# Performance work log

Hardware: AMD Instinct MI355X
Metric: run time of the kernel (lower is better)

The kernel has to match this reference:

```python
import jax, jax.numpy as jnp
import numpy as np

N_NODES = 50000
N_EDGES = 800000
HC = 64      # hidden_channels
NG = 5       # num_gaussians
NF = 64      # num_filters
SL = 20      # short_len
NC = 2       # n_conv
Z_DIM = 2 * NF + SL  # 148
BN_EPS = 1e-5


def setup_inputs() -> dict:
    key = jax.random.key(0)
    ks = jax.random.split(key, 16)
    s = 0.05
    return {
        "h": jax.random.normal(ks[0], (N_NODES, HC), dtype=jnp.float32),
        "edge_index": jax.random.randint(ks[1], (2, N_EDGES), 0, N_NODES, dtype=jnp.int32),
        "edge_weight": jax.random.uniform(ks[2], (N_EDGES,), dtype=jnp.float32),
        "edge_attr": jax.random.uniform(ks[3], (N_EDGES, NG), dtype=jnp.float32),
        "lin0_w": jax.random.normal(ks[4], (HC, NF), dtype=jnp.float32) * s,
        "lin0_b": jnp.zeros((NF,), dtype=jnp.float32),
        "short_w": jax.random.normal(ks[5], (NG, SL), dtype=jnp.float32) * s,
        "short_b": jnp.zeros((SL,), dtype=jnp.float32),
        "linf_w": jax.random.normal(ks[6], (NC, Z_DIM, NF), dtype=jnp.float32) * s,
        "linf_b": jnp.zeros((NC, NF), dtype=jnp.float32),
        "lins_w": jax.random.normal(ks[7], (NC, Z_DIM, NF), dtype=jnp.float32) * s,
        "lins_b": jnp.zeros((NC, NF), dtype=jnp.float32),
        "bn_gamma": jnp.ones((NC, NF), dtype=jnp.float32),
        "bn_beta": jnp.zeros((NC, NF), dtype=jnp.float32),
        "data": 0,
    }


def reference(h, edge_index, edge_weight, edge_attr,
              lin0_w, lin0_b, short_w, short_b,
              linf_w, linf_b, lins_w, lins_b,
              bn_gamma, bn_beta, data):
    # lin0 + relu
    out = jax.nn.relu(h @ lin0_w + lin0_b)                      # [N, NF]
    # short edge-attr projection + relu
    ea = jax.nn.relu(edge_attr @ short_w + short_b)             # [E, SL]
    src = edge_index[0]  # x_j (source)
    dst = edge_index[1]  # x_i (target / aggregation index)
    n = out.shape[0]
    for l in range(NC):
        x_i = out[dst]                                          # [E, NF]
        x_j = out[src]                                          # [E, NF]
        z = jnp.concatenate([x_i, x_j, ea], axis=-1)            # [E, 148]
        msg = jax.nn.sigmoid(z @ linf_w[l] + linf_b[l]) * \
              jax.nn.softplus(z @ lins_w[l] + lins_b[l])        # [E, NF]
        agg = jax.ops.segment_sum(msg, dst, num_segments=n)     # [N, NF]
        # BatchNorm1d (training-mode batch stats, biased variance)
        mean = jnp.mean(agg, axis=0)
        var = jnp.mean((agg - mean) ** 2, axis=0)
        bn = (agg - mean) * jax.lax.rsqrt(var + BN_EPS) * bn_gamma[l] + bn_beta[l]
        conv_out = bn + out                                     # CGConv internal residual
        out = out + jax.nn.relu(conv_out)                       # _Interactions residual
    return out
```

## Files before the change

kernel.cpp:

```cpp
#include <hip/hip_runtime.h>
#include <hip/hip_bf16.h>

#define N_NODES 50000
#define N_EDGES 800000
#define SCAN_NB 49
#define EPW 32
#define EW_BLOCKS 6250

typedef __hip_bfloat16 bf16;
typedef unsigned int u32;
typedef unsigned short u16;
typedef _Float16 hh2 __attribute__((ext_vector_type(2)));

#if defined(__has_builtin)
#if __has_builtin(__builtin_amdgcn_fdot2)
#define HAVE_FDOT2 1
#endif
#endif

__device__ __forceinline__ float bfb(u32 b) { return __uint_as_float(b << 16); }

__device__ __forceinline__ u16 f2bf(float x) {
    bf16 a = __float2bfloat16(x);
    u16 u;
    __builtin_memcpy(&u, &a, 2);
    return u;
}

__device__ __forceinline__ hh2 pkrtz(float a, float b) {
    auto r = __builtin_amdgcn_cvt_pkrtz(a, b);
    hh2 o;
    __builtin_memcpy(&o, &r, 4);
    return o;
}

__device__ __forceinline__ float ldf(const void* p, long i, int f32) {
    if (f32) return ((const float*)p)[i];
    return bfb((u32)((const u16*)p)[i]);
}

__device__ __forceinline__ int detect_f32(const u32* g) { return g[0] == 0x3F800000u; }

__global__ __launch_bounds__(256) void k_front(const void* __restrict__ h,
        const void* __restrict__ w, const void* __restrict__ b,
        const u32* __restrict__ gr, u16* __restrict__ outw,
        const int* __restrict__ ei, int* __restrict__ cnt,
        int* __restrict__ tsum, u32* __restrict__ aggz) {
    int t = threadIdx.x;
    for (int i = blockIdx.x * 256 + t; i < N_NODES * 64; i += 1024 * 256)
        aggz[i] = 0;
    if (blockIdx.x >= 512) {
        __shared__ int lts[SCAN_NB];
        if (t < SCAN_NB) lts[t] = 0;
        __syncthreads();
        int bid = blockIdx.x - 512;
        for (int e = bid * 256 + t; e < N_EDGES; e += 512 * 256) {
            int dst = ei[N_EDGES + e];
            atomicAdd(&cnt[dst], 1);
            atomicAdd(&lts[dst >> 10], 1);
        }
        __syncthreads();
        if (t < SCAN_NB) atomicAdd(&tsum[t], lts[t]);
        return;
    }
    __shared__ float Wl[64 * 64];
    __shared__ float bl[64];
    __shared__ float hs[256];
    int f32 = detect_f32(gr);
    for (int i = t; i < 4096; i += 256) Wl[i] = ldf(w, i, f32);
    if (t < 64) bl[t] = ldf(b, t, f32);
    int c = t & 63, g = t >> 6;
    for (int chunk = blockIdx.x; chunk < N_NODES / 4; chunk += 512) {
        __syncthreads();
        int node0 = chunk * 4;
        hs[t] = ldf(h, (long)node0 * 64 + t, f32);
        __syncthreads();
        float acc = bl[c];
        #pragma unroll
        for (int k = 0; k < 64; ++k) acc = fmaf(hs[g * 64 + k], Wl[k * 64 + c], acc);
        outw[(node0 + g) * 64 + c] = f2bf(fmaxf(acc, 0.f));
    }
}

__global__ __launch_bounds__(1024) void k_scan(int* __restrict__ cnt,
        const int* __restrict__ tsum) {
    __shared__ int wsum[16];
    __shared__ int boff_s;
    int t = threadIdx.x, lane = t & 63, wv = t >> 6;
    if (wv == 0) {
        int v = (lane < SCAN_NB && lane < (int)blockIdx.x) ? tsum[lane] : 0;
        #pragma unroll
        for (int d = 32; d >= 1; d >>= 1) v += __shfl_xor(v, d, 64);
        if (lane == 0) boff_s = v;
    }
    int i = blockIdx.x * 1024 + t;
    int v = (i < N_NODES) ? cnt[i] : 0;
    int incl = v;
    #pragma unroll
    for (int d = 1; d < 64; d <<= 1) {
        int x = __shfl_up(incl, d, 64);
        if (lane >= d) incl += x;
    }
    if (lane == 63) wsum[wv] = incl;
    __syncthreads();
    if (wv == 0) {
        int s = (lane < 16) ? wsum[lane] : 0;
        int si = s;
        #pragma unroll
        for (int d = 1; d < 16; d <<= 1) {
            int x = __shfl_up(si, d, 64);
            if (lane >= d) si += x;
        }
        if (lane < 16) wsum[lane] = si - s;
    }
    __syncthreads();
    incl += wsum[wv] + boff_s;
    if (i < N_NODES) cnt[i] = incl - v;
}

__global__ __launch_bounds__(256) void k_pproj_bin(const u16* __restrict__ outw,
        const void* __restrict__ linf_w, const void* __restrict__ lins_w,
        const void* __restrict__ linf_b, const void* __restrict__ lins_b,
        const u32* __restrict__ gr, bf16* __restrict__ P,
        const int* __restrict__ ei, int* __restrict__ cursor,
        u32* __restrict__ bpack, const void* __restrict__ eattr,
        const void* __restrict__ short_w, const void* __restrict__ short_b,
        u32* __restrict__ sea) {
    int t = threadIdx.x;
    int f32 = detect_f32(gr);
    if (blockIdx.x >= 512) {
        __shared__ float swl[100];
        __shared__ float sbl[20];
        if (t < 100) swl[t] = ldf(short_w, t, f32);
        if (t < 20) sbl[t] = ldf(short_b, t, f32);
        __syncthreads();
        int bid = blockIdx.x - 512;
        for (int e = bid * 256 + t; e < N_EDGES; e += 512 * 256) {
            int dst = ei[N_EDGES + e];
            int src = ei[e];
            int slot = atomicAdd(&cursor[dst], 1);
            bpack[slot] = ((u32)dst << 16) | (u32)src;
            float a0 = ldf(eattr, (long)e * 5 + 0, f32);
            float a1 = ldf(eattr, (long)e * 5 + 1, f32);
            float a2 = ldf(eattr, (long)e * 5 + 2, f32);
            float a3 = ldf(eattr, (long)e * 5 + 3, f32);
            float a4 = ldf(eattr, (long)e * 5 + 4, f32);
            u32* sp = sea + (size_t)slot * 10u;
            #pragma unroll
            for (int j = 0; j < 10; ++j) {
                float e0 = sbl[2 * j], e1 = sbl[2 * j + 1];
                e0 = fmaf(a0, swl[0 * 20 + 2 * j], e0);
                e1 = fmaf(a0, swl[0 * 20 + 2 * j + 1], e1);
                e0 = fmaf(a1, swl[1 * 20 + 2 * j], e0);
                e1 = fmaf(a1, swl[1 * 20 + 2 * j + 1], e1);
                e0 = fmaf(a2, swl[2 * 20 + 2 * j], e0);
                e1 = fmaf(a2, swl[2 * 20 + 2 * j + 1], e1);
                e0 = fmaf(a3, swl[3 * 20 + 2 * j], e0);
                e1 = fmaf(a3, swl[3 * 20 + 2 * j + 1], e1);
                e0 = fmaf(a4, swl[4 * 20 + 2 * j], e0);
                e1 = fmaf(a4, swl[4 * 20 + 2 * j + 1], e1);
                e0 = fmaxf(e0, 0.f);
                e1 = fmaxf(e1, 0.f);
                hh2 h2 = pkrtz(e0, e1);
                u32 u;
                __builtin_memcpy(&u, &h2, 4);
                sp[j] = u;
            }
        }
        return;
    }
    int b = t >> 6, c = t & 63;
    const void* wmat = (b < 2) ? linf_w : lins_w;
    long woff = (long)(b & 1) * 4096;
    float bias = 0.f;
    if (b == 0) bias = ldf(linf_b, c, f32);
    if (b == 2) bias = ldf(lins_b, c, f32);
    float wc[64];
    #pragma unroll
    for (int k = 0; k < 64; ++k) wc[k] = ldf(wmat, woff + k * 64 + c, f32);
    int stidx = (b & 1) * 128 + 2 * c + (b >> 1);
    __shared__ float hs[16 * 64];
    for (int chunk = blockIdx.x; chunk < N_NODES / 16; chunk += 512) {
        __syncthreads();
        int node0 = chunk * 16;
        for (int i = t; i < 1024; i += 256) hs[i] = bfb((u32)outw[node0 * 64 + i]);
        __syncthreads();
        for (int n = 0; n < 16; ++n) {
            float acc = bias;
            #pragma unroll
            for (int k = 0; k < 64; ++k) acc = fmaf(hs[n * 64 + k], wc[k], acc);
            P[(size_t)(node0 + n) * 256 + stidx] = __float2bfloat16(acc);
        }
    }
}

struct EB { u32 ea; u32 pd[4]; u32 ps[4]; int d[4]; };

__global__ __launch_bounds__(256) void k_edge_flat(const u32* __restrict__ bpack,
        const u32* __restrict__ sea,
        const void* __restrict__ linf_w, const void* __restrict__ lins_w,
        const u32* __restrict__ gr, int layer,
        const u32* __restrict__ Pw, float* __restrict__ agg) {
    int f32 = detect_f32(gr);
    int t = threadIdx.x, lane = t & 63, wv = t >> 6;
    int wid = blockIdx.x * 4 + wv;
    int base = wid * EPW;

    int eo = (lane / 10) & 3, j10 = lane % 10;
    long wbase = (long)layer * 9472 + 8192;
    hh2 wf2[10], ws2[10];
    #pragma unroll
    for (int j = 0; j < 10; ++j) {
        wf2[j] = pkrtz(ldf(linf_w, wbase + (2 * j) * 64 + lane, f32),
                       ldf(linf_w, wbase + (2 * j + 1) * 64 + lane, f32));
        ws2[j] = pkrtz(ldf(lins_w, wbase + (2 * j) * 64 + lane, f32),
                       ldf(lins_w, wbase + (2 * j + 1) * 64 + lane, f32));
    }

    float acc = 0.f;
    int cur = -1;

    auto issueA = [&](u32& Apk, int b) {
        Apk = bpack[(u32)base + 4u * (u32)b + ((u32)lane & 3u)];
    };
    auto issueB = [&](EB& B, u32 Apk, int b) {
        B.ea = sea[(u32)(base + 4 * b + eo) * 10u + (u32)j10];
        #pragma unroll
        for (int i = 0; i < 4; ++i) {
            u32 pki = (u32)__builtin_amdgcn_readlane((int)Apk, i);
            int d = (int)(pki >> 16);
            u32 s = pki & 0xFFFFu;
            B.d[i] = d;
            B.pd[i] = Pw[(u32)d * 128u + (u32)lane];
            B.ps[i] = Pw[s * 128u + 64u + (u32)lane];
        }
    };
    auto computeC = [&](const EB& B) {
        #pragma unroll
        for (int i = 0; i < 4; ++i) {
            int d = B.d[i];
            u32 pd = B.pd[i], ps = B.ps[i];
            float f = bfb(pd & 0xFFFFu) + bfb(ps & 0xFFFFu);
            float s = __uint_as_float(pd & 0xFFFF0000u) +
                      __uint_as_float(ps & 0xFFFF0000u);
            #pragma unroll
            for (int j = 0; j < 10; ++j) {
                u32 u = (u32)__builtin_amdgcn_readlane((int)B.ea, 10 * i + j);
                hh2 hu;
                __builtin_memcpy(&hu, &u, 4);
#ifdef HAVE_FDOT2
                f = __builtin_amdgcn_fdot2(hu, wf2[j], f, false);
                s = __builtin_amdgcn_fdot2(hu, ws2[j], s, false);
#else
                f = fmaf((float)hu[0], (float)wf2[j][0], f);
                f = fmaf((float)hu[1], (float)wf2[j][1], f);
                s = fmaf((float)hu[0], (float)ws2[j][0], s);
                s = fmaf((float)hu[1], (float)ws2[j][1], s);
#endif
            }
            float sig = 1.f / (1.f + __expf(-f));
            float sp = fmaxf(s, 0.f) + __logf(1.f + __expf(-fabsf(s)));
            if (d != cur) {
                if (cur >= 0)
                    atomicAdd(agg + (u32)cur * 64u + (u32)lane, acc);
                acc = 0.f;
                cur = d;
            }
            acc += sig * sp;
        }
    };

    u32 A0, A1, A2, A3;
    EB B0, B1, B2, B3;
    issueA(A0, 0); issueA(A1, 1); issueA(A2, 2); issueA(A3, 3);
    issueB(B0, A0, 0); issueB(B1, A1, 1); issueB(B2, A2, 2);
    issueA(A0, 4); issueB(B3, A3, 3); computeC(B0);
    issueA(A1, 5); issueB(B0, A0, 4); computeC(B1);
    issueA(A2, 6); issueB(B1, A1, 5); computeC(B2);
    issueA(A3, 7); issueB(B2, A2, 6); computeC(B3);
    issueB(B3, A3, 7); computeC(B0);
    computeC(B1);
    computeC(B2);
    computeC(B3);
    if (cur >= 0) atomicAdd(agg + (u32)cur * 64u + (u32)lane, acc);
}

__global__ __launch_bounds__(256) void k_stats(const float* __restrict__ aggf,
        float* __restrict__ stats) {
    int t = threadIdx.x, c = t & 63, r = t >> 6;
    float s = 0.f, s2 = 0.f;
    for (int row = blockIdx.x * 4 + r; row < N_NODES; row += gridDim.x * 4) {
        float v = aggf[row * 64 + c];
        s += v;
        s2 = fmaf(v, v, s2);
    }
    __shared__ float red[512];
    red[r * 64 + c] = s;
    red[256 + r * 64 + c] = s2;
    __syncthreads();
    if (t < 64) {
        atomicAdd(&stats[t], red[t] + red[64 + t] + red[128 + t] + red[192 + t]);
    } else if (t < 128) {
        int cc = t - 64;
        atomicAdd(&stats[64 + cc],
                  red[256 + cc] + red[320 + cc] + red[384 + cc] + red[448 + cc]);
    }
}

__global__ __launch_bounds__(256) void k_apply_pproj(float* __restrict__ aggf,
        const float* __restrict__ stats, const void* __restrict__ gamma,
        const void* __restrict__ beta, const u32* __restrict__ gr,
        u16* __restrict__ outw,
        const void* __restrict__ linf_w, const void* __restrict__ lins_w,
        const void* __restrict__ linf_b, const void* __restrict__ lins_b,
        bf16* __restrict__ P) {
    int f32 = detect_f32(gr);
    int t = threadIdx.x;
    int b = t >> 6, c = t & 63;
    const float invN = 1.f / (float)N_NODES;
    float mean = stats[c] * invN;
    float var = fmaxf(stats[64 + c] * invN - mean * mean, 0.f);
    float inv = rsqrtf(var + 1e-5f);
    float g = ldf(gamma, c, f32);
    float be = ldf(beta, c, f32);
    const void* wmat = (b < 2) ? linf_w : lins_w;
    long woff = 9472 + (long)(b & 1) * 4096;
    float bias = 0.f;
    if (b == 0) bias = ldf(linf_b, 64 + c, f32);
    if (b == 2) bias = ldf(lins_b, 64 + c, f32);
    float wc[64];
    #pragma unroll
    for (int k = 0; k < 64; ++k) wc[k] = ldf(wmat, woff + k * 64 + c, f32);
    int stidx = (b & 1) * 128 + 2 * c + (b >> 1);
    __shared__ float hs[16 * 64];
    for (int chunk = blockIdx.x; chunk < N_NODES / 16; chunk += 512) {
        __syncthreads();
        int node0 = chunk * 16;
        #pragma unroll
        for (int q = 0; q < 4; ++q) {
            int idx = node0 * 64 + q * 256 + t;
            float o = bfb((u32)outw[idx]);
            float a = aggf[idx];
            float bn = fmaf((a - mean) * inv, g, be);
            float no = o + fmaxf(bn + o, 0.f);
            outw[idx] = f2bf(no);
            aggf[idx] = 0.f;
            hs[q * 256 + t] = no;
        }
        __syncthreads();
        for (int n = 0; n < 16; ++n) {
            float acc = bias;
            #pragma unroll
            for (int k = 0; k < 64; ++k) acc = fmaf(hs[n * 64 + k], wc[k], acc);
            P[(size_t)(node0 + n) * 256 + stidx] = __float2bfloat16(acc);
        }
    }
}

__global__ __launch_bounds__(256) void k_apply_final(const float* __restrict__ aggf,
        const float* __restrict__ stats, const void* __restrict__ gamma,
        const void* __restrict__ beta, const u32* __restrict__ gr,
        const u16* __restrict__ outw, void* __restrict__ dout) {
    int f32 = detect_f32(gr);
    const float invN = 1.f / (float)N_NODES;
    for (int idx = blockIdx.x * 256 + threadIdx.x; idx < N_NODES * 64;
         idx += gridDim.x * 256) {
        int c = idx & 63;
        float mean = stats[c] * invN;
        float var = fmaxf(stats[64 + c] * invN - mean * mean, 0.f);
        float inv = rsqrtf(var + 1e-5f);
        float o = bfb((u32)outw[idx]);
        float a = aggf[idx];
        float g = ldf(gamma, 64 + c, f32);
        float be = ldf(beta, 64 + c, f32);
        float bn = fmaf((a - mean) * inv, g, be);
        float no = o + fmaxf(bn + o, 0.f);
        if (f32) ((float*)dout)[idx] = no;
        else ((bf16*)dout)[idx] = __float2bfloat16(no);
    }
}

extern "C" void kernel_launch(void* const* d_in, const int* in_sizes, int n_in,
                              void* d_out, int out_size, void* d_ws, size_t ws_size,
                              hipStream_t stream) {
    const void* h       = d_in[0];
    const int*  ei      = (const int*)d_in[1];
    const void* eattr   = d_in[3];
    const void* lin0_w  = d_in[4];
    const void* lin0_b  = d_in[5];
    const void* short_w = d_in[6];
    const void* short_b = d_in[7];
    const void* linf_w  = d_in[8];
    const void* linf_b  = d_in[9];
    const void* lins_w  = d_in[10];
    const void* lins_b  = d_in[11];
    const void* gamma   = d_in[12];
    const void* beta    = d_in[13];
    const u32*  gr      = (const u32*)gamma;

    u16*   outw  = (u16*)d_ws;
    bf16*  P     = (bf16*)(outw + (size_t)N_NODES * 64);
    u32*   bpack = (u32*)(P + (size_t)N_NODES * 256);
    float* aggf  = (float*)(bpack + N_EDGES);
    int*   cnt   = (int*)(aggf + (size_t)N_NODES * 64);
    float* stats = (float*)(cnt + N_NODES);
    int*   tsum  = (int*)(stats + 256);
    u32*   sea   = (u32*)(tsum + 64);

    size_t zbytes = (size_t)N_NODES * 4 + 256 * 4 + 64 * 4;
    (void)hipMemsetAsync(cnt, 0, zbytes, stream);

    k_front<<<1024, 256, 0, stream>>>(h, lin0_w, lin0_b, gr, outw, ei, cnt,
                                      tsum, (u32*)aggf);
    k_scan<<<SCAN_NB, 1024, 0, stream>>>(cnt, tsum);
    k_pproj_bin<<<1024, 256, 0, stream>>>(outw, linf_w, lins_w, linf_b, lins_b,
                                          gr, P, ei, cnt, bpack, eattr,
                                          short_w, short_b, sea);
    k_edge_flat<<<EW_BLOCKS, 256, 0, stream>>>(bpack, sea, linf_w, lins_w, gr, 0,
                                               (const u32*)P, aggf);
    k_stats<<<256, 256, 0, stream>>>(aggf, stats);
    k_apply_pproj<<<512, 256, 0, stream>>>(aggf, stats, gamma, beta, gr, outw,
                                           linf_w, lins_w, linf_b, lins_b, P);
    k_edge_flat<<<EW_BLOCKS, 256, 0, stream>>>(bpack, sea, linf_w, lins_w, gr, 1,
                                               (const u32*)P, aggf);
    k_stats<<<256, 256, 0, stream>>>(aggf, stats + 128);
    k_apply_final<<<1024, 256, 0, stream>>>(aggf, stats + 128, gamma, beta, gr,
                                            outw, d_out);
}
```

Measured before the change: 463.7 us.

## Vectorize elementwise kernels, prepack edge weights, shrink edges per wave

Several changes land together. Edge kernel: edges per wave drop from 32 to 20 with more blocks, the software pipeline is shortened to match, and the short-feature weights are prepacked once into fp16 pairs in workspace so each wave loads them with five 16-byte reads instead of many scalar loads and conversions. The stats, apply and final kernels switch to float4/ushort4 vectorized accesses, the aggregate zeroing uses uint4 stores, and lin0 processes 16 nodes per chunk. The aim is fewer memory transactions and less per-wave setup, at the cost of more waves, more atomic flushes and an extra workspace buffer whose prepack is written by one block of the binning kernel.

```diff
diff --git a/kernel.cpp b/kernel.cpp
--- a/kernel.cpp
+++ b/kernel.cpp
@@ -4,8 +4,8 @@
 #define N_NODES 50000
 #define N_EDGES 800000
 #define SCAN_NB 49
-#define EPW 32
-#define EW_BLOCKS 6250
+#define EPW 20
+#define EW_BLOCKS 10000
 
 typedef __hip_bfloat16 bf16;
 typedef unsigned int u32;
@@ -45,10 +45,11 @@
         const void* __restrict__ w, const void* __restrict__ b,
         const u32* __restrict__ gr, u16* __restrict__ outw,
         const int* __restrict__ ei, int* __restrict__ cnt,
-        int* __restrict__ tsum, u32* __restrict__ aggz) {
+        int* __restrict__ tsum, uint4* __restrict__ aggz4) {
     int t = threadIdx.x;
-    for (int i = blockIdx.x * 256 + t; i < N_NODES * 64; i += 1024 * 256)
-        aggz[i] = 0;
+    uint4 z4 = {0u, 0u, 0u, 0u};
+    for (int i = blockIdx.x * 256 + t; i < N_NODES * 16; i += 1024 * 256)
+        aggz4[i] = z4;
     if (blockIdx.x >= 512) {
         __shared__ int lts[SCAN_NB];
         if (t < SCAN_NB) lts[t] = 0;
@@ -65,20 +66,24 @@
     }
     __shared__ float Wl[64 * 64];
     __shared__ float bl[64];
-    __shared__ float hs[256];
+    __shared__ float hs[16 * 64];
     int f32 = detect_f32(gr);
     for (int i = t; i < 4096; i += 256) Wl[i] = ldf(w, i, f32);
     if (t < 64) bl[t] = ldf(b, t, f32);
     int c = t & 63, g = t >> 6;
-    for (int chunk = blockIdx.x; chunk < N_NODES / 4; chunk += 512) {
-        __syncthreads();
-        int node0 = chunk * 4;
-        hs[t] = ldf(h, (long)node0 * 64 + t, f32);
-        __syncthreads();
-        float acc = bl[c];
-        #pragma unroll
-        for (int k = 0; k < 64; ++k) acc = fmaf(hs[g * 64 + k], Wl[k * 64 + c], acc);
-        outw[(node0 + g) * 64 + c] = f2bf(fmaxf(acc, 0.f));
+    for (int chunk = blockIdx.x; chunk < N_NODES / 16; chunk += 512) {
+        __syncthreads();
+        int node0 = chunk * 16;
+        for (int i = t; i < 1024; i += 256) hs[i] = ldf(h, (long)node0 * 64 + i, f32);
+        __syncthreads();
+        #pragma unroll
+        for (int nn = 0; nn < 4; ++nn) {
+            int n = g * 4 + nn;
+            float acc = bl[c];
+            #pragma unroll
+            for (int k = 0; k < 64; ++k) acc = fmaf(hs[n * 64 + k], Wl[k * 64 + c], acc);
+            outw[(node0 + n) * 64 + c] = f2bf(fmaxf(acc, 0.f));
+        }
     }
 }
 
@@ -125,10 +130,27 @@
         const int* __restrict__ ei, int* __restrict__ cursor,
         u32* __restrict__ bpack, const void* __restrict__ eattr,
         const void* __restrict__ short_w, const void* __restrict__ short_b,
-        u32* __restrict__ sea) {
+        u32* __restrict__ sea, u32* __restrict__ wpk) {
     int t = threadIdx.x;
     int f32 = detect_f32(gr);
     if (blockIdx.x >= 512) {
+        if (blockIdx.x == 512 && t < 128) {
+            int ly = t >> 6, ln = t & 63;
+            long wb = (long)ly * 9472 + 8192;
+            u32* wp = wpk + (size_t)(ly * 64 + ln) * 20;
+            #pragma unroll
+            for (int j = 0; j < 10; ++j) {
+                hh2 fp = pkrtz(ldf(linf_w, wb + (2 * j) * 64 + ln, f32),
+                               ldf(linf_w, wb + (2 * j + 1) * 64 + ln, f32));
+                hh2 sp = pkrtz(ldf(lins_w, wb + (2 * j) * 64 + ln, f32),
+                               ldf(lins_w, wb + (2 * j + 1) * 64 + ln, f32));
+                u32 uf, us;
+                __builtin_memcpy(&uf, &fp, 4);
+                __builtin_memcpy(&us, &sp, 4);
+                wp[2 * j] = uf;
+                wp[2 * j + 1] = us;
+            }
+        }
         __shared__ float swl[100];
         __shared__ float sbl[20];
         if (t < 100) swl[t] = ldf(short_w, t, f32);
@@ -183,7 +205,13 @@
     for (int chunk = blockIdx.x; chunk < N_NODES / 16; chunk += 512) {
         __syncthreads();
         int node0 = chunk * 16;
-        for (int i = t; i < 1024; i += 256) hs[i] = bfb((u32)outw[node0 * 64 + i]);
+        {
+            ushort4 hv = *(const ushort4*)(outw + (size_t)node0 * 64 + t * 4);
+            hs[t * 4 + 0] = bfb((u32)hv.x);
+            hs[t * 4 + 1] = bfb((u32)hv.y);
+            hs[t * 4 + 2] = bfb((u32)hv.z);
+            hs[t * 4 + 3] = bfb((u32)hv.w);
+        }
         __syncthreads();
         for (int n = 0; n < 16; ++n) {
             float acc = bias;
@@ -197,24 +225,23 @@
 struct EB { u32 ea; u32 pd[4]; u32 ps[4]; int d[4]; };
 
 __global__ __launch_bounds__(256) void k_edge_flat(const u32* __restrict__ bpack,
-        const u32* __restrict__ sea,
-        const void* __restrict__ linf_w, const void* __restrict__ lins_w,
-        const u32* __restrict__ gr, int layer,
+        const u32* __restrict__ sea, const u32* __restrict__ wpk, int layer,
         const u32* __restrict__ Pw, float* __restrict__ agg) {
-    int f32 = detect_f32(gr);
     int t = threadIdx.x, lane = t & 63, wv = t >> 6;
     int wid = blockIdx.x * 4 + wv;
     int base = wid * EPW;
 
     int eo = (lane / 10) & 3, j10 = lane % 10;
-    long wbase = (long)layer * 9472 + 8192;
+    const uint4* wv4 = (const uint4*)(wpk + (size_t)(layer * 64 + lane) * 20);
+    uint4 q0 = wv4[0], q1 = wv4[1], q2 = wv4[2], q3 = wv4[3], q4 = wv4[4];
+    u32 wbuf[20] = {q0.x, q0.y, q0.z, q0.w, q1.x, q1.y, q1.z, q1.w,
+                    q2.x, q2.y, q2.z, q2.w, q3.x, q3.y, q3.z, q3.w,
+                    q4.x, q4.y, q4.z, q4.w};
     hh2 wf2[10], ws2[10];
     #pragma unroll
     for (int j = 0; j < 10; ++j) {
-        wf2[j] = pkrtz(ldf(linf_w, wbase + (2 * j) * 64 + lane, f32),
-                       ldf(linf_w, wbase + (2 * j + 1) * 64 + lane, f32));
-        ws2[j] = pkrtz(ldf(lins_w, wbase + (2 * j) * 64 + lane, f32),
-                       ldf(lins_w, wbase + (2 * j + 1) * 64 + lane, f32));
+        __builtin_memcpy(&wf2[j], &wbuf[2 * j], 4);
+        __builtin_memcpy(&ws2[j], &wbuf[2 * j + 1], 4);
     }
 
     float acc = 0.f;
@@ -274,36 +301,41 @@
     EB B0, B1, B2, B3;
     issueA(A0, 0); issueA(A1, 1); issueA(A2, 2); issueA(A3, 3);
     issueB(B0, A0, 0); issueB(B1, A1, 1); issueB(B2, A2, 2);
-    issueA(A0, 4); issueB(B3, A3, 3); computeC(B0);
-    issueA(A1, 5); issueB(B0, A0, 4); computeC(B1);
-    issueA(A2, 6); issueB(B1, A1, 5); computeC(B2);
-    issueA(A3, 7); issueB(B2, A2, 6); computeC(B3);
-    issueB(B3, A3, 7); computeC(B0);
+    issueA(A0, 4);
+    issueB(B3, A3, 3);
+    computeC(B0);
+    issueB(B0, A0, 4);
     computeC(B1);
     computeC(B2);
     computeC(B3);
+    computeC(B0);
     if (cur >= 0) atomicAdd(agg + (u32)cur * 64u + (u32)lane, acc);
 }
 
 __global__ __launch_bounds__(256) void k_stats(const float* __restrict__ aggf,
         float* __restrict__ stats) {
-    int t = threadIdx.x, c = t & 63, r = t >> 6;
-    float s = 0.f, s2 = 0.f;
-    for (int row = blockIdx.x * 4 + r; row < N_NODES; row += gridDim.x * 4) {
-        float v = aggf[row * 64 + c];
-        s += v;
-        s2 = fmaf(v, v, s2);
-    }
-    __shared__ float red[512];
-    red[r * 64 + c] = s;
-    red[256 + r * 64 + c] = s2;
+    int t = threadIdx.x;
+    int r = t >> 4, c4 = (t & 15) * 4;
+    float s0 = 0.f, s1 = 0.f, s2 = 0.f, s3 = 0.f;
+    float q0 = 0.f, q1 = 0.f, q2 = 0.f, q3 = 0.f;
+    for (int row = blockIdx.x * 16 + r; row < N_NODES; row += 256 * 16) {
+        float4 v = *(const float4*)(aggf + (size_t)row * 64 + c4);
+        s0 += v.x; s1 += v.y; s2 += v.z; s3 += v.w;
+        q0 = fmaf(v.x, v.x, q0); q1 = fmaf(v.y, v.y, q1);
+        q2 = fmaf(v.z, v.z, q2); q3 = fmaf(v.w, v.w, q3);
+    }
+    __shared__ float red[2][16][64];
+    red[0][r][c4 + 0] = s0; red[0][r][c4 + 1] = s1;
+    red[0][r][c4 + 2] = s2; red[0][r][c4 + 3] = s3;
+    red[1][r][c4 + 0] = q0; red[1][r][c4 + 1] = q1;
+    red[1][r][c4 + 2] = q2; red[1][r][c4 + 3] = q3;
     __syncthreads();
-    if (t < 64) {
-        atomicAdd(&stats[t], red[t] + red[64 + t] + red[128 + t] + red[192 + t]);
-    } else if (t < 128) {
-        int cc = t - 64;
-        atomicAdd(&stats[64 + cc],
-                  red[256 + cc] + red[320 + cc] + red[384 + cc] + red[448 + cc]);
+    if (t < 128) {
+        int m = t >> 6, c = t & 63;
+        float a = 0.f;
+        #pragma unroll
+        for (int k = 0; k < 16; ++k) a += red[m][k][c];
+        atomicAdd(&stats[m * 64 + c], a);
     }
 }
 
@@ -317,12 +349,18 @@
     int f32 = detect_f32(gr);
     int t = threadIdx.x;
     int b = t >> 6, c = t & 63;
+    int nid = t >> 4, c4 = (t & 15) * 4;
     const float invN = 1.f / (float)N_NODES;
-    float mean = stats[c] * invN;
-    float var = fmaxf(stats[64 + c] * invN - mean * mean, 0.f);
-    float inv = rsqrtf(var + 1e-5f);
-    float g = ldf(gamma, c, f32);
-    float be = ldf(beta, c, f32);
+    float m4[4], iv4[4], g4[4], b4[4];
+    #pragma unroll
+    for (int k = 0; k < 4; ++k) {
+        float mean = stats[c4 + k] * invN;
+        float var = fmaxf(stats[64 + c4 + k] * invN - mean * mean, 0.f);
+        m4[k] = mean;
+        iv4[k] = rsqrtf(var + 1e-5f);
+        g4[k] = ldf(gamma, c4 + k, f32);
+        b4[k] = ldf(beta, c4 + k, f32);
+    }
     const void* wmat = (b < 2) ? linf_w : lins_w;
     long woff = 9472 + (long)(b & 1) * 4096;
     float bias = 0.f;
@@ -336,16 +374,25 @@
     for (int chunk = blockIdx.x; chunk < N_NODES / 16; chunk += 512) {
         __syncthreads();
         int node0 = chunk * 16;
-        #pragma unroll
-        for (int q = 0; q < 4; ++q) {
-            int idx = node0 * 64 + q * 256 + t;
-            float o = bfb((u32)outw[idx]);
-            float a = aggf[idx];
-            float bn = fmaf((a - mean) * inv, g, be);
-            float no = o + fmaxf(bn + o, 0.f);
-            outw[idx] = f2bf(no);
-            aggf[idx] = 0.f;
-            hs[q * 256 + t] = no;
+        {
+            size_t idx = (size_t)(node0 + nid) * 64 + c4;
+            float4 a = *(const float4*)(aggf + idx);
+            ushort4 ow = *(const ushort4*)(outw + idx);
+            const float* ap = (const float*)&a;
+            const u16* op = (const u16*)&ow;
+            float no[4];
+            #pragma unroll
+            for (int k = 0; k < 4; ++k) {
+                float o = bfb((u32)op[k]);
+                float bn = fmaf((ap[k] - m4[k]) * iv4[k], g4[k], b4[k]);
+                no[k] = o + fmaxf(bn + o, 0.f);
+            }
+            ushort4 nw = {f2bf(no[0]), f2bf(no[1]), f2bf(no[2]), f2bf(no[3])};
+            *(ushort4*)(outw + idx) = nw;
+            float4 z4 = {0.f, 0.f, 0.f, 0.f};
+            *(float4*)(aggf + idx) = z4;
+            float4 hv = {no[0], no[1], no[2], no[3]};
+            *(float4*)(&hs[nid * 64 + c4]) = hv;
         }
         __syncthreads();
         for (int n = 0; n < 16; ++n) {
@@ -363,20 +410,37 @@
         const u16* __restrict__ outw, void* __restrict__ dout) {
     int f32 = detect_f32(gr);
     const float invN = 1.f / (float)N_NODES;
-    for (int idx = blockIdx.x * 256 + threadIdx.x; idx < N_NODES * 64;
-         idx += gridDim.x * 256) {
-        int c = idx & 63;
-        float mean = stats[c] * invN;
-        float var = fmaxf(stats[64 + c] * invN - mean * mean, 0.f);
-        float inv = rsqrtf(var + 1e-5f);
-        float o = bfb((u32)outw[idx]);
-        float a = aggf[idx];
-        float g = ldf(gamma, 64 + c, f32);
-        float be = ldf(beta, 64 + c, f32);
-        float bn = fmaf((a - mean) * inv, g, be);
-        float no = o + fmaxf(bn + o, 0.f);
-        if (f32) ((float*)dout)[idx] = no;
-        else ((bf16*)dout)[idx] = __float2bfloat16(no);
+    int t0 = blockIdx.x * 256 + threadIdx.x;
+    int c4 = (t0 & 15) * 4;
+    float m4[4], iv4[4], g4[4], b4[4];
+    #pragma unroll
+    for (int k = 0; k < 4; ++k) {
+        float mean = stats[c4 + k] * invN;
+        float var = fmaxf(stats[64 + c4 + k] * invN - mean * mean, 0.f);
+        m4[k] = mean;
+        iv4[k] = rsqrtf(var + 1e-5f);
+        g4[k] = ldf(gamma, 64 + c4 + k, f32);
+        b4[k] = ldf(beta, 64 + c4 + k, f32);
+    }
+    for (int i4 = t0; i4 < N_NODES * 16; i4 += 1024 * 256) {
+        float4 a = *(const float4*)(aggf + (size_t)i4 * 4);
+        ushort4 ow = *(const ushort4*)(outw + (size_t)i4 * 4);
+        const float* ap = (const float*)&a;
+        const u16* op = (const u16*)&ow;
+        float no[4];
+        #pragma unroll
+        for (int k = 0; k < 4; ++k) {
+            float o = bfb((u32)op[k]);
+            float bn = fmaf((ap[k] - m4[k]) * iv4[k], g4[k], b4[k]);
+            no[k] = o + fmaxf(bn + o, 0.f);
+        }
+        if (f32) {
+            float4 o4 = {no[0], no[1], no[2], no[3]};
+            *(float4*)((float*)dout + (size_t)i4 * 4) = o4;
+        } else {
+            ushort4 o4 = {f2bf(no[0]), f2bf(no[1]), f2bf(no[2]), f2bf(no[3])};
+            *(ushort4*)((u16*)dout + (size_t)i4 * 4) = o4;
+        }
     }
 }
 
@@ -406,22 +470,23 @@
     float* stats = (float*)(cnt + N_NODES);
     int*   tsum  = (int*)(stats + 256);
     u32*   sea   = (u32*)(tsum + 64);
+    u32*   wpk   = sea + (size_t)N_EDGES * 10;
 
     size_t zbytes = (size_t)N_NODES * 4 + 256 * 4 + 64 * 4;
     (void)hipMemsetAsync(cnt, 0, zbytes, stream);
 
     k_front<<<1024, 256, 0, stream>>>(h, lin0_w, lin0_b, gr, outw, ei, cnt,
-                                      tsum, (u32*)aggf);
+                                      tsum, (uint4*)aggf);
     k_scan<<<SCAN_NB, 1024, 0, stream>>>(cnt, tsum);
     k_pproj_bin<<<1024, 256, 0, stream>>>(outw, linf_w, lins_w, linf_b, lins_b,
                                           gr, P, ei, cnt, bpack, eattr,
-                                          short_w, short_b, sea);
-    k_edge_flat<<<EW_BLOCKS, 256, 0, stream>>>(bpack, sea, linf_w, lins_w, gr, 0,
+                                          short_w, short_b, sea, wpk);
+    k_edge_flat<<<EW_BLOCKS, 256, 0, stream>>>(bpack, sea, wpk, 0,
                                                (const u32*)P, aggf);
     k_stats<<<256, 256, 0, stream>>>(aggf, stats);
     k_apply_pproj<<<512, 256, 0, stream>>>(aggf, stats, gamma, beta, gr, outw,
                                            linf_w, lins_w, linf_b, lins_b, P);
-    k_edge_flat<<<EW_BLOCKS, 256, 0, stream>>>(bpack, sea, linf_w, lins_w, gr, 1,
+    k_edge_flat<<<EW_BLOCKS, 256, 0, stream>>>(bpack, sea, wpk, 1,
                                                (const u32*)P, aggf);
     k_stats<<<256, 256, 0, stream>>>(aggf, stats + 128);
     k_apply_final<<<1024, 256, 0, stream>>>(aggf, stats + 128, gamma, beta, gr,
```

Result: faster. 442.3 us (-4.6%).
